# Optimization experiments

Measured on AMD Instinct MI355X. Metric: run time of the kernel, lower is better.

Reference implementation:

```python
import jax, jax.numpy as jnp
import numpy as np
from jax import lax

BN_EPS = 1e-5

def _maxpool3(x):
    # F.max_pool2d(x, 3, stride=1, padding=1): pads with -inf, window 3x3
    return lax.reduce_window(x, -jnp.inf, lax.max, (1, 1, 3, 3), (1, 1, 1, 1), 'SAME')

def _conv(x, w):
    return lax.conv_general_dilated(x, w, (1, 1), 'SAME',
                                    dimension_numbers=('NCHW', 'OIHW', 'NCHW'))

def _bn(x, g, b, m, v):
    inv = lax.rsqrt(v + BN_EPS)
    return (x - m[None, :, None, None]) * (g * inv)[None, :, None, None] + b[None, :, None, None]


def setup_inputs() -> dict:
    key = jax.random.key(0)
    ks = jax.random.split(key, 12)
    B, C, H, W = 8, 128, 160, 160
    c_ = 64  # int(c2 * 0.5)
    x = jax.random.normal(ks[0], (B, C, H, W), jnp.float32)
    fill_strength_raw = jnp.full((1, C, 1, 1), 0.5, jnp.float32)
    w1 = jax.random.normal(ks[1], (c_, C, 1, 1), jnp.float32) * 0.05
    w2 = jax.random.normal(ks[2], (c_, c_, 3, 3), jnp.float32) * 0.05
    w3 = jax.random.normal(ks[3], (C, c_, 1, 1), jnp.float32) * 0.05
    def bn_params(k, ch):
        k1, k2, k3 = jax.random.split(k, 3)
        return (jnp.ones((ch,), jnp.float32),
                jnp.zeros((ch,), jnp.float32),
                jax.random.normal(k1, (ch,), jnp.float32) * 0.1,
                jax.random.uniform(k2, (ch,), jnp.float32, 0.5, 1.5))
    g1, b1, m1, v1 = bn_params(ks[4], c_)
    g2, b2, m2, v2 = bn_params(ks[5], c_)
    g3, b3, m3, v3 = bn_params(ks[6], C)
    return dict(x=x, fill_strength_raw=fill_strength_raw,
                w1=w1, g1=g1, b1=b1, m1=m1, v1=v1,
                w2=w2, g2=g2, b2=b2, m2=m2, v2=v2,
                w3=w3, g3=g3, b3=b3, m3=m3, v3=v3)


def reference(x, fill_strength_raw,
              w1, g1, b1, m1, v1,
              w2, g2, b2, m2, v2,
              w3, g3, b3, m3, v3):
    bg_thresh_ratio, ch_sharp, ch_thresh, edge_sharp, edge_thresh = 0.3, 3.0, 0.3, 5.0, 0.5
    # AdaptiveBackgroundFill
    baseline = jnp.min(x, axis=(2, 3), keepdims=True)            # [B,C,1,1]
    local_contrast = _maxpool3(x) + _maxpool3(-x)                # max_s - min_s
    mean_contrast = jnp.mean(local_contrast, axis=(2, 3), keepdims=True) + 1e-6
    bg_mask = (local_contrast < bg_thresh_ratio * mean_contrast).astype(x.dtype)
    strength = jax.nn.sigmoid(fill_strength_raw)
    filled = x * (1.0 - strength * bg_mask) + baseline * strength * bg_mask
    # ChannelAwareEdgeEnhance_Attn
    x_abs = jnp.abs(filled)
    max_ch = jnp.max(x_abs, axis=(2, 3), keepdims=True)
    avg_ch = jnp.mean(x_abs, axis=(2, 3), keepdims=True)
    ch_weight = jax.nn.sigmoid(ch_sharp * (max_ch - avg_ch - ch_thresh))
    x_spatial = jnp.mean(x_abs, axis=1, keepdims=True)           # [B,1,H,W]
    edge = _maxpool3(x_spatial) + _maxpool3(-x_spatial)
    edge_weight = jax.nn.sigmoid(edge_sharp * (edge - edge_thresh))
    enhanced = filled * ch_weight * (1.0 + edge_weight)
    # DenseBottleneck (n=1, shortcut, c1==c2) with inference-mode BatchNorm
    o = jax.nn.silu(_bn(_conv(enhanced, w1), g1, b1, m1, v1))
    o = jax.nn.silu(_bn(_conv(o, w2), g2, b2, m2, v2))
    o = _bn(_conv(o, w3), g3, b3, m3, v3)
    out = jax.nn.silu(o + enhanced)
    # proj is Identity since c1 == c2
    return out
```

## Files before the change

### kernel.cpp

```cpp
#include <hip/hip_runtime.h>
#include <math.h>

#define BB 8
#define CC 128
#define CH 64
#define HH 160
#define WW 160
#define HW (HH*WW)
#define PP 162
#define INF __builtin_inff()

typedef __bf16 bfv8 __attribute__((ext_vector_type(8)));
typedef __bf16 bfv4 __attribute__((ext_vector_type(4)));
typedef __bf16 bfv2 __attribute__((ext_vector_type(2)));
typedef float  f4   __attribute__((ext_vector_type(4)));

__device__ __forceinline__ float sgm(float z){ return 1.0f/(1.0f + __expf(-z)); }
__device__ __forceinline__ float silu_(float z){ return z/(1.0f + __expf(-z)); }
__device__ __forceinline__ f4 MFMA(bfv8 a, bfv8 b, f4 c){
  return __builtin_amdgcn_mfma_f32_16x16x32_bf16(a, b, c, 0, 0, 0);
}

__global__ __launch_bounds__(256) void kprep2(const float* __restrict__ w1,
                                              const float* __restrict__ g1, const float* __restrict__ b1,
                                              const float* __restrict__ m1, const float* __restrict__ v1,
                                              const float* __restrict__ w2,
                                              const float* __restrict__ g2, const float* __restrict__ b2,
                                              const float* __restrict__ m2, const float* __restrict__ v2,
                                              const float* __restrict__ w3,
                                              const float* __restrict__ g3, const float* __restrict__ b3,
                                              const float* __restrict__ m3, const float* __restrict__ v3,
                                              __bf16* __restrict__ w1b, __bf16* __restrict__ w2b,
                                              __bf16* __restrict__ w3b, float* __restrict__ scsh,
                                              __bf16* __restrict__ o1p){
  int bid = blockIdx.x;
  if(bid < 64){
    int t = bid*256 + threadIdx.x;
    int stride = 64*256;
    for(int i=t; i<CH*CC; i+=stride) w1b[i] = (__bf16)w1[i];
    for(int i=t; i<CC*CH; i+=stride) w3b[i] = (__bf16)w3[i];
    for(int i=t; i<9*CH*CH; i+=stride){
      int tap = i >> 12; int rem = i & 4095; int oc = rem >> 6; int ic = rem & 63;
      w2b[i] = (__bf16)w2[(oc*CH + ic)*9 + tap];
    }
    if(t < CH){
      float s = g1[t]*rsqrtf(v1[t] + 1e-5f);
      scsh[t] = s; scsh[64+t] = b1[t] - m1[t]*s;
      float s2 = g2[t]*rsqrtf(v2[t] + 1e-5f);
      scsh[128+t] = s2; scsh[192+t] = b2[t] - m2[t]*s2;
    }
    if(t >= 64 && t < 64+CC){
      int c = t - 64;
      float s3 = g3[c]*rsqrtf(v3[c] + 1e-5f);
      scsh[256+c] = s3; scsh[384+c] = b3[c] - m3[c]*s3;
    }
  } else {
    int b = bid - 64;
    __bf16* base = o1p + (size_t)b*PP*PP*CH;
    int t = threadIdx.x;
    bfv4 z = {(__bf16)0.f,(__bf16)0.f,(__bf16)0.f,(__bf16)0.f};
    for(int i=t; i<644*16; i+=256){
      int e = i >> 4; int c4 = (i & 15)*4;
      int h, w;
      if(e < 162){ h = 0; w = e; }
      else if(e < 324){ h = 161; w = e - 162; }
      else if(e < 484){ h = e - 324 + 1; w = 0; }
      else { h = e - 484 + 1; w = 161; }
      *(bfv4*)(base + ((size_t)h*PP + w)*CH + c4) = z;
    }
  }
}

__device__ __forceinline__ void load8s(const float* __restrict__ xp, int lc,
                                       int start, float (&C)[8]){
  #pragma unroll
  for(int k=0;k<8;++k){
    int hr = start + k;
    C[k] = (hr < HH) ? xp[hr*WW + lc] : 0.f;
  }
}

__device__ __forceinline__ void proc1s(int base, const float (&C)[8],
                                       float& Mp, float& mp, float& Mc, float& mc,
                                       float& mn, float& sum){
  #pragma unroll
  for(int k=0;k<8;++k){
    int hr = base + 1 + k;
    float Lv = __shfl_up(C[k],1), Rv = __shfl_down(C[k],1);
    float Mn, mr;
    if(hr < HH){
      Mn = fmaxf(fmaxf(Lv,C[k]),Rv);
      mr = fminf(fminf(Lv,C[k]),Rv);
      mn = fminf(mn, C[k]);
    } else { Mn = -INF; mr = INF; }
    sum += fmaxf(fmaxf(Mp,Mc),Mn) - fminf(fminf(mp,mc),mr);
    Mp=Mc; mp=mc; Mc=Mn; mc=mr;
  }
}

__device__ __forceinline__ void proc2s(int base, int lc, bool act, const float (&C)[8],
                                       float& Mp, float& mp, float& Mc, float& mc,
                                       float& cen, float& amax, float& asum,
                                       float th, float basev, float s,
                                       __bf16* __restrict__ fp){
  #pragma unroll
  for(int k=0;k<8;++k){
    int hr = base + 1 + k;
    int h  = base + k;
    float Lv = __shfl_up(C[k],1), Rv = __shfl_down(C[k],1);
    float Mn, mr;
    if(hr < HH){
      Mn = fmaxf(fmaxf(Lv,C[k]),Rv);
      mr = fminf(fminf(Lv,C[k]),Rv);
    } else { Mn = -INF; mr = INF; }
    float contrast = fmaxf(fmaxf(Mp,Mc),Mn) - fminf(fminf(mp,mc),mr);
    float f = (contrast < th) ? cen*(1.f-s) + basev*s : cen;
    if(act) fp[h*WW + lc] = (__bf16)f;
    float a = fabsf(f);
    amax = fmaxf(amax, a); asum += a;
    Mp=Mc; mp=mc; Mc=Mn; mc=mr; cen = C[k];
  }
}

__global__ __launch_bounds__(192) void k12(const float* __restrict__ x,
                                           const float* __restrict__ fsr,
                                           __bf16* __restrict__ fill16,
                                           float* __restrict__ chw){
  __shared__ float ra[256], rb[256];
  __shared__ float sb[2];
  int bc = blockIdx.x;
  int c  = bc & (CC-1);
  int t  = threadIdx.x;
  int w  = t >> 6, l = t & 63;
  int oc = 62*w + l - 1;
  bool act = (l >= 1) && (l <= 62) && (oc < WW);
  int lc = oc < 0 ? 0 : (oc > WW-1 ? WW-1 : oc);
  const float* xp = x + (size_t)bc*HW;

  float CA[8], CB[8];

  float mn = INF, sum = 0.f;
  float Mp=-INF, mp=INF, Mc, mc;
  {
    float C0 = xp[lc];
    float Lv = __shfl_up(C0,1), Rv = __shfl_down(C0,1);
    Mc = fmaxf(fmaxf(Lv,C0),Rv); mc = fminf(fminf(Lv,C0),Rv);
    mn = C0;
  }
  load8s(xp, lc, 1, CA);
  for(int h0=0; h0<HH; h0+=16){
    load8s(xp, lc, h0+9, CB);
    proc1s(h0,   CA, Mp, mp, Mc, mc, mn, sum);
    if(h0+16 < HH) load8s(xp, lc, h0+17, CA);
    proc1s(h0+8, CB, Mp, mp, Mc, mc, mn, sum);
  }
  ra[t] = act ? mn : INF;
  rb[t] = act ? sum : 0.f;
  if(t < 64){ ra[192+t] = INF; rb[192+t] = 0.f; }
  __syncthreads();
  for(int s=128; s>0; s>>=1){
    if(t < s){ ra[t]=fminf(ra[t],ra[t+s]); rb[t]+=rb[t+s]; }
    __syncthreads();
  }
  if(t==0){ sb[0]=ra[0]; sb[1]=0.3f*(rb[0]/(float)HW + 1e-6f); }
  __syncthreads();
  float base = sb[0], th = sb[1];
  float s = sgm(fsr[c]);

  __bf16* fp = fill16 + (size_t)bc*HW;
  float amax=0.f, asum=0.f;
  Mp=-INF; mp=INF;
  float cen;
  {
    float C0 = xp[lc];
    float Lv = __shfl_up(C0,1), Rv = __shfl_down(C0,1);
    Mc = fmaxf(fmaxf(Lv,C0),Rv); mc = fminf(fminf(Lv,C0),Rv);
    cen = C0;
  }
  load8s(xp, lc, 1, CA);
  for(int h0=0; h0<HH; h0+=16){
    load8s(xp, lc, h0+9, CB);
    proc2s(h0,   lc, act, CA, Mp, mp, Mc, mc, cen, amax, asum, th, base, s, fp);
    if(h0+16 < HH) load8s(xp, lc, h0+17, CA);
    proc2s(h0+8, lc, act, CB, Mp, mp, Mc, mc, cen, amax, asum, th, base, s, fp);
  }
  ra[t] = act ? amax : 0.f;
  rb[t] = act ? asum : 0.f;
  if(t < 64){ ra[192+t] = 0.f; rb[192+t] = 0.f; }
  __syncthreads();
  for(int st=128; st>0; st>>=1){
    if(t < st){ ra[t]=fmaxf(ra[t],ra[t+st]); rb[t]+=rb[t+st]; }
    __syncthreads();
  }
  if(t==0) chw[bc] = sgm(3.0f*(ra[0] - rb[0]/(float)HW - 0.3f));
}

__global__ __launch_bounds__(64) void k3_xs(const __bf16* __restrict__ fill16,
                                            float* __restrict__ xs){
  int i = blockIdx.x*64 + threadIdx.x;
  int b = i / (HW/8); int p8 = (i - b*(HW/8))*8;
  const __bf16* fp = fill16 + (size_t)b*CC*HW + p8;
  float s0=0,s1=0,s2=0,s3=0,s4=0,s5=0,s6=0,s7=0;
  #pragma unroll 4
  for(int c=0; c<CC; ++c){
    bfv8 v = *(const bfv8*)(fp + (size_t)c*HW);
    s0 += fabsf((float)v[0]); s1 += fabsf((float)v[1]);
    s2 += fabsf((float)v[2]); s3 += fabsf((float)v[3]);
    s4 += fabsf((float)v[4]); s5 += fabsf((float)v[5]);
    s6 += fabsf((float)v[6]); s7 += fabsf((float)v[7]);
  }
  f4 r0 = {s0*(1.f/CC), s1*(1.f/CC), s2*(1.f/CC), s3*(1.f/CC)};
  f4 r1 = {s4*(1.f/CC), s5*(1.f/CC), s6*(1.f/CC), s7*(1.f/CC)};
  *(f4*)(xs + (size_t)b*HW + p8)     = r0;
  *(f4*)(xs + (size_t)b*HW + p8 + 4) = r1;
}

__global__ __launch_bounds__(256) void k_enh(const __bf16* __restrict__ fill16,
                                             const float* __restrict__ chw,
                                             const float* __restrict__ xs,
                                             __bf16* __restrict__ enh){
  __shared__ __bf16 tile[64][132];
  __shared__ float ewl[64];
  int b  = blockIdx.x / 400;
  int p0 = (blockIdx.x % 400) * 64;
  int t  = threadIdx.x;
  if(t < 64){
    int p = p0 + t; int h = p/WW, w = p - h*WW;
    const float* xpb = xs + (size_t)b*HW;
    int h0 = h>0?h-1:0, h1 = h<HH-1?h+1:h;
    int w0 = w>0?w-1:0, w1 = w<WW-1?w+1:w;
    float M = -INF, m = INF;
    for(int hh=h0; hh<=h1; ++hh)
      for(int ww=w0; ww<=w1; ++ww){
        float v = xpb[hh*WW+ww]; M = fmaxf(M,v); m = fminf(m,v);
      }
    ewl[t] = sgm(5.0f*((M-m) - 0.5f));
  }
  __syncthreads();
  #pragma unroll
  for(int e=0; e<8; ++e){
    int idx = e*256 + t; int ic = idx >> 4; int pp = (idx & 15)*4;
    bfv4 v = *(const bfv4*)(fill16 + ((size_t)(b*CC + ic))*HW + p0 + pp);
    float g = chw[b*CC + ic];
    #pragma unroll
    for(int i2=0;i2<4;++i2)
      tile[pp+i2][ic] = (__bf16)((float)v[i2] * g * (1.f + ewl[pp+i2]));
  }
  __syncthreads();
  #pragma unroll
  for(int e=0; e<8; ++e){
    int idx = e*256 + t; int p = idx >> 5; int icg = idx & 31;
    bfv4 v = *(const bfv4*)&tile[p][icg*4];
    *(bfv4*)&enh[((size_t)(b*HW + p0 + p))*CC + icg*4] = v;
  }
}

__global__ __launch_bounds__(256) void c1_mfma(const __bf16* __restrict__ enh,
                                               const __bf16* __restrict__ w1b,
                                               const float* __restrict__ scsh,
                                               __bf16* __restrict__ o1p){
  int lane = threadIdx.x & 63, wv = threadIdx.x >> 6;
  int u = blockIdx.x*4 + wv;
  int b = u / 320; int r = u % 320; int h = r >> 1; int w0base = (r & 1)*80;
  int q = lane >> 4, j = lane & 15;
  bfv8 afr[4][4];
  #pragma unroll
  for(int mt=0; mt<4; ++mt)
    #pragma unroll
    for(int kk=0; kk<4; ++kk)
      afr[mt][kk] = *(const bfv8*)&w1b[(mt*16 + j)*CC + kk*32 + q*8];
  f4 sc4[4], sh4[4];
  #pragma unroll
  for(int mt=0; mt<4; ++mt){
    sc4[mt] = *(const f4*)&scsh[mt*16 + q*4];
    sh4[mt] = *(const f4*)&scsh[64 + mt*16 + q*4];
  }
  const __bf16* ebase = enh + (size_t)b*HW*CC;
  __bf16* obase = o1p + (size_t)b*PP*PP*CH;
  for(int s5=0; s5<5; ++s5){
    int w0 = w0base + s5*16;
    int p0 = h*WW + w0;
    const __bf16* bp = ebase + (size_t)(p0 + j)*CC + q*8;
    bfv8 bf[4];
    #pragma unroll
    for(int kk=0; kk<4; ++kk) bf[kk] = *(const bfv8*)(bp + kk*32);
    f4 acc[4] = {{0,0,0,0},{0,0,0,0},{0,0,0,0},{0,0,0,0}};
    #pragma unroll
    for(int kk=0; kk<4; ++kk)
      #pragma unroll
      for(int mt=0; mt<4; ++mt)
        acc[mt] = MFMA(afr[mt][kk], bf[kk], acc[mt]);
    int w = w0 + j;
    __bf16* op = obase + ((size_t)(h+1)*PP + (w+1))*CH + q*4;
    #pragma unroll
    for(int mt=0; mt<4; ++mt){
      bfv4 ov;
      #pragma unroll
      for(int rr=0; rr<4; ++rr){
        float z = acc[mt][rr]*sc4[mt][rr] + sh4[mt][rr];
        ov[rr] = (__bf16)silu_(z);
      }
      *(bfv4*)(op + mt*16) = ov;
    }
  }
}

__global__ __launch_bounds__(256) void c2_mfma(const __bf16* __restrict__ o1p,
                                               const __bf16* __restrict__ w2b,
                                               const float* __restrict__ scsh,
                                               __bf16* __restrict__ o2){
  __shared__ __bf16 lds[4*82*64];
  int lane = threadIdx.x & 63, mt = threadIdx.x >> 6;
  int u = blockIdx.x;
  int b = u / 160; int r_ = u % 160; int hp = r_ >> 1; int wh = r_ & 1;
  int h0 = hp*2;
  int wstart = wh*80;
  int q = lane >> 4, j = lane & 15;
  const __bf16* ibase = o1p + (size_t)b*PP*PP*CH;
  {
    int t = threadIdx.x;
    int wvbase = t & ~63;
    #pragma unroll
    for(int it=0; it<11; ++it){
      int i = it*256 + t;
      if(i < 2624){
        int r = i / 656; int rem = i - r*656;
        int w = rem >> 3; int kp = rem & 7;
        int k = kp ^ (w & 7);
        const __bf16* src = ibase + ((size_t)(h0+r)*PP + wstart + w)*CH + k*8;
        char* dst = (char*)lds + (size_t)(it*256 + wvbase)*16;
        __builtin_amdgcn_global_load_lds((const __attribute__((address_space(1))) void*)src,
                                         (__attribute__((address_space(3))) void*)dst,
                                         16, 0, 0);
      }
    }
  }
  bfv8 afr[9][2];
  #pragma unroll
  for(int t=0; t<9; ++t)
    #pragma unroll
    for(int icb=0; icb<2; ++icb)
      afr[t][icb] = *(const bfv8*)&w2b[(t*CH + mt*16 + j)*CH + icb*32 + q*8];
  f4 sc4 = *(const f4*)&scsh[128 + mt*16 + q*4];
  f4 sh4 = *(const f4*)&scsh[192 + mt*16 + q*4];
  asm volatile("s_waitcnt vmcnt(0)" ::: "memory");
  __syncthreads();

  __bf16* obase = o2 + (size_t)b*HW*CH;
  for(int s5=0; s5<5; ++s5){
    int wb = s5*16;
    f4 a00={0,0,0,0}, a01={0,0,0,0}, a10={0,0,0,0}, a11={0,0,0,0};
    #pragma unroll
    for(int r=0; r<4; ++r){
      bfv8 bv0[3], bv1[3];
      #pragma unroll
      for(int dw=0; dw<3; ++dw){
        int wl = wb + j + dw;
        int basee = r*5248 + wl*64;
        int k0 = q ^ (wl & 7);
        bv0[dw] = *(const bfv8*)&lds[basee + k0*8];
        bv1[dw] = *(const bfv8*)&lds[basee + (k0^4)*8];
      }
      #pragma unroll
      for(int dw=0; dw<3; ++dw){
        if(r < 3){
          a00 = MFMA(afr[r*3+dw][0], bv0[dw], a00);
          a01 = MFMA(afr[r*3+dw][1], bv1[dw], a01);
        }
        if(r >= 1){
          a10 = MFMA(afr[(r-1)*3+dw][0], bv0[dw], a10);
          a11 = MFMA(afr[(r-1)*3+dw][1], bv1[dw], a11);
        }
      }
    }
    f4 acc0 = a00 + a01, acc1 = a10 + a11;
    int w0 = wstart + wb;
    __bf16* op0 = obase + ((size_t)(h0*WW + w0 + j))*CH + mt*16 + q*4;
    __bf16* op1 = obase + ((size_t)((h0+1)*WW + w0 + j))*CH + mt*16 + q*4;
    bfv4 ov0, ov1;
    #pragma unroll
    for(int rr=0; rr<4; ++rr){
      ov0[rr] = (__bf16)silu_(acc0[rr]*sc4[rr] + sh4[rr]);
      ov1[rr] = (__bf16)silu_(acc1[rr]*sc4[rr] + sh4[rr]);
    }
    *(bfv4*)op0 = ov0;
    *(bfv4*)op1 = ov1;
  }
}

__global__ __launch_bounds__(256) void c3_mfma(const __bf16* __restrict__ o2,
                                               const __bf16* __restrict__ w3b,
                                               const float* __restrict__ scsh,
                                               const __bf16* __restrict__ enh,
                                               float* __restrict__ out){
  __shared__ float ot[CC][66];
  int lane = threadIdx.x & 63, wv = threadIdx.x >> 6;
  int b = blockIdx.x / 400; int p0 = (blockIdx.x % 400)*64;
  int q = lane >> 4, j = lane & 15;
  int px0 = wv*16;
  int pix = p0 + px0 + j;
  const __bf16* bp = o2 + ((size_t)b*HW + pix)*CH + q*8;
  bfv8 bf0 = *(const bfv8*)bp;
  bfv8 bf1 = *(const bfv8*)(bp + 32);
  f4 acc[8];
  #pragma unroll
  for(int mt=0; mt<8; ++mt){
    bfv8 a0 = *(const bfv8*)&w3b[(mt*16 + j)*CH + q*8];
    bfv8 a1 = *(const bfv8*)&w3b[(mt*16 + j)*CH + 32 + q*8];
    f4 z = {0.f,0.f,0.f,0.f};
    z = MFMA(a0, bf0, z);
    z = MFMA(a1, bf1, z);
    acc[mt] = z;
  }
  const __bf16* ep = enh + ((size_t)b*HW + pix)*CC;
  #pragma unroll
  for(int mt=0; mt<8; ++mt){
    f4 scg = *(const f4*)&scsh[256 + mt*16 + q*4];
    f4 shg = *(const f4*)&scsh[384 + mt*16 + q*4];
    bfv4 e4 = *(const bfv4*)(ep + mt*16 + q*4);
    #pragma unroll
    for(int rr=0; rr<4; ++rr){
      float z = acc[mt][rr]*scg[rr] + shg[rr] + (float)e4[rr];
      ot[mt*16 + q*4 + rr][px0 + j] = silu_(z);
    }
  }
  __syncthreads();
  int t = threadIdx.x;
  #pragma unroll
  for(int e=0; e<8; ++e){
    int oc = e*16 + (t >> 4);
    int c4 = (t & 15)*4;
    f4 v = *(const f4*)&ot[oc][c4];
    *(f4*)&out[((size_t)(b*CC + oc))*HW + p0 + c4] = v;
  }
}

extern "C" void kernel_launch(void* const* d_in, const int* in_sizes, int n_in,
                              void* d_out, int out_size, void* d_ws, size_t ws_size,
                              hipStream_t stream) {
  const float* x   = (const float*)d_in[0];
  const float* fsr = (const float*)d_in[1];
  const float* w1  = (const float*)d_in[2];
  const float* g1  = (const float*)d_in[3];
  const float* b1  = (const float*)d_in[4];
  const float* m1  = (const float*)d_in[5];
  const float* v1  = (const float*)d_in[6];
  const float* w2  = (const float*)d_in[7];
  const float* g2  = (const float*)d_in[8];
  const float* b2  = (const float*)d_in[9];
  const float* m2  = (const float*)d_in[10];
  const float* v2  = (const float*)d_in[11];
  const float* w3  = (const float*)d_in[12];
  const float* g3  = (const float*)d_in[13];
  const float* b3  = (const float*)d_in[14];
  const float* m3  = (const float*)d_in[15];
  const float* v3  = (const float*)d_in[16];
  float* out = (float*)d_out;

  char* wp = (char*)d_ws;
  __bf16* fill16 = (__bf16*)wp;  wp += (size_t)BB*CC*HW*2;
  __bf16* enh    = (__bf16*)wp;  wp += (size_t)BB*HW*CC*2;
  __bf16* o1p    = (__bf16*)wp;  wp += (size_t)BB*PP*PP*CH*2;
  __bf16* o2b    = (__bf16*)wp;  wp += (size_t)BB*HW*CH*2;
  float*  xs     = (float*)wp;   wp += (size_t)BB*HW*4;
  float*  chw    = (float*)wp;   wp += 1024*4;
  __bf16* w1b    = (__bf16*)wp;  wp += (size_t)CH*CC*2;
  __bf16* w3b    = (__bf16*)wp;  wp += (size_t)CC*CH*2;
  __bf16* w2b    = (__bf16*)wp;  wp += (size_t)9*CH*CH*2;
  float*  scsh   = (float*)wp;   wp += 512*4;

  kprep2  <<<dim3(72), dim3(256), 0, stream>>>(w1,g1,b1,m1,v1, w2,g2,b2,m2,v2,
                                               w3,g3,b3,m3,v3, w1b,w2b,w3b,scsh, o1p);
  k12     <<<dim3(BB*CC), dim3(192), 0, stream>>>(x, fsr, fill16, chw);
  k3_xs   <<<dim3(400), dim3(64), 0, stream>>>(fill16, xs);
  k_enh   <<<dim3(BB*400), dim3(256), 0, stream>>>(fill16, chw, xs, enh);
  c1_mfma <<<dim3(640), dim3(256), 0, stream>>>(enh, w1b, scsh, o1p);
  c2_mfma <<<dim3(1280), dim3(256), 0, stream>>>(o1p, w2b, scsh, o2b);
  c3_mfma <<<dim3(3200), dim3(256), 0, stream>>>(o2b, w3b, scsh, enh, out);
}
```

Baseline: 193.5 us.

## Fuse enhance into conv1, recompute residual in conv3, precompute edge weights

```diff
diff --git a/kernel.cpp b/kernel.cpp
--- a/kernel.cpp
+++ b/kernel.cpp
@@ -12,13 +12,21 @@
 
 typedef __bf16 bfv8 __attribute__((ext_vector_type(8)));
 typedef __bf16 bfv4 __attribute__((ext_vector_type(4)));
-typedef __bf16 bfv2 __attribute__((ext_vector_type(2)));
 typedef float  f4   __attribute__((ext_vector_type(4)));
 
 __device__ __forceinline__ float sgm(float z){ return 1.0f/(1.0f + __expf(-z)); }
 __device__ __forceinline__ float silu_(float z){ return z/(1.0f + __expf(-z)); }
 __device__ __forceinline__ f4 MFMA(bfv8 a, bfv8 b, f4 c){
   return __builtin_amdgcn_mfma_f32_16x16x32_bf16(a, b, c, 0, 0, 0);
+}
+
+__device__ __forceinline__ float hrow3L(const float* __restrict__ r, int w,
+                                        float& hM, float& hm){
+  float cv = r[w];
+  float M = cv, m = cv;
+  if(w > 0){ float l = r[w-1]; M = fmaxf(M,l); m = fminf(m,l); }
+  if(w < WW-1){ float rr = r[w+1]; M = fmaxf(M,rr); m = fminf(m,rr); }
+  hM = M; hm = m; return cv;
 }
 
 __global__ __launch_bounds__(256) void kprep2(const float* __restrict__ w1,
@@ -215,27 +223,38 @@
   *(f4*)(xs + (size_t)b*HW + p8 + 4) = r1;
 }
 
-__global__ __launch_bounds__(256) void k_enh(const __bf16* __restrict__ fill16,
-                                             const float* __restrict__ chw,
-                                             const float* __restrict__ xs,
-                                             __bf16* __restrict__ enh){
+__global__ __launch_bounds__(256) void k4_ew(const float* __restrict__ xs,
+                                             float* __restrict__ ew){
+  int b  = blockIdx.x / 5;
+  int r0 = (blockIdx.x % 5) * 32;
+  int w  = threadIdx.x;
+  if(w >= WW) return;
+  const float* xp = xs + (size_t)b*HW;
+  float* ep = ew + (size_t)b*HW;
+  float hMp, hmp, hMc, hmc, hMn, hmn;
+  if(r0 > 0) hrow3L(xp + (r0-1)*WW, w, hMp, hmp); else { hMp=-INF; hmp=INF; }
+  hrow3L(xp + r0*WW, w, hMc, hmc);
+  #pragma unroll 4
+  for(int h=r0; h<r0+32; ++h){
+    if(h < HH-1) hrow3L(xp + (h+1)*WW, w, hMn, hmn); else { hMn=-INF; hmn=INF; }
+    float contrast = fmaxf(fmaxf(hMp,hMc),hMn) - fminf(fminf(hmp,hmc),hmn);
+    ep[h*WW + w] = sgm(5.0f*(contrast - 0.5f));
+    hMp=hMc; hmp=hmc; hMc=hMn; hmc=hmn;
+  }
+}
+
+__global__ __launch_bounds__(256) void c1f(const __bf16* __restrict__ fill16,
+                                           const float* __restrict__ chw,
+                                           const float* __restrict__ ew,
+                                           const __bf16* __restrict__ w1b,
+                                           const float* __restrict__ scsh,
+                                           __bf16* __restrict__ o1p){
   __shared__ __bf16 tile[64][132];
   __shared__ float ewl[64];
   int b  = blockIdx.x / 400;
   int p0 = (blockIdx.x % 400) * 64;
   int t  = threadIdx.x;
-  if(t < 64){
-    int p = p0 + t; int h = p/WW, w = p - h*WW;
-    const float* xpb = xs + (size_t)b*HW;
-    int h0 = h>0?h-1:0, h1 = h<HH-1?h+1:h;
-    int w0 = w>0?w-1:0, w1 = w<WW-1?w+1:w;
-    float M = -INF, m = INF;
-    for(int hh=h0; hh<=h1; ++hh)
-      for(int ww=w0; ww<=w1; ++ww){
-        float v = xpb[hh*WW+ww]; M = fmaxf(M,v); m = fminf(m,v);
-      }
-    ewl[t] = sgm(5.0f*((M-m) - 0.5f));
-  }
+  if(t < 64) ewl[t] = ew[(size_t)b*HW + p0 + t];
   __syncthreads();
   #pragma unroll
   for(int e=0; e<8; ++e){
@@ -246,22 +265,7 @@
     for(int i2=0;i2<4;++i2)
       tile[pp+i2][ic] = (__bf16)((float)v[i2] * g * (1.f + ewl[pp+i2]));
   }
-  __syncthreads();
-  #pragma unroll
-  for(int e=0; e<8; ++e){
-    int idx = e*256 + t; int p = idx >> 5; int icg = idx & 31;
-    bfv4 v = *(const bfv4*)&tile[p][icg*4];
-    *(bfv4*)&enh[((size_t)(b*HW + p0 + p))*CC + icg*4] = v;
-  }
-}
-
-__global__ __launch_bounds__(256) void c1_mfma(const __bf16* __restrict__ enh,
-                                               const __bf16* __restrict__ w1b,
-                                               const float* __restrict__ scsh,
-                                               __bf16* __restrict__ o1p){
-  int lane = threadIdx.x & 63, wv = threadIdx.x >> 6;
-  int u = blockIdx.x*4 + wv;
-  int b = u / 320; int r = u % 320; int h = r >> 1; int w0base = (r & 1)*80;
+  int lane = t & 63, wv = t >> 6;
   int q = lane >> 4, j = lane & 15;
   bfv8 afr[4][4];
   #pragma unroll
@@ -275,33 +279,28 @@
     sc4[mt] = *(const f4*)&scsh[mt*16 + q*4];
     sh4[mt] = *(const f4*)&scsh[64 + mt*16 + q*4];
   }
-  const __bf16* ebase = enh + (size_t)b*HW*CC;
-  __bf16* obase = o1p + (size_t)b*PP*PP*CH;
-  for(int s5=0; s5<5; ++s5){
-    int w0 = w0base + s5*16;
-    int p0 = h*WW + w0;
-    const __bf16* bp = ebase + (size_t)(p0 + j)*CC + q*8;
-    bfv8 bf[4];
-    #pragma unroll
-    for(int kk=0; kk<4; ++kk) bf[kk] = *(const bfv8*)(bp + kk*32);
-    f4 acc[4] = {{0,0,0,0},{0,0,0,0},{0,0,0,0},{0,0,0,0}};
-    #pragma unroll
-    for(int kk=0; kk<4; ++kk)
-      #pragma unroll
-      for(int mt=0; mt<4; ++mt)
-        acc[mt] = MFMA(afr[mt][kk], bf[kk], acc[mt]);
-    int w = w0 + j;
-    __bf16* op = obase + ((size_t)(h+1)*PP + (w+1))*CH + q*4;
-    #pragma unroll
-    for(int mt=0; mt<4; ++mt){
-      bfv4 ov;
-      #pragma unroll
-      for(int rr=0; rr<4; ++rr){
-        float z = acc[mt][rr]*sc4[mt][rr] + sh4[mt][rr];
-        ov[rr] = (__bf16)silu_(z);
-      }
-      *(bfv4*)(op + mt*16) = ov;
-    }
+  __syncthreads();
+  bfv8 bf[4];
+  #pragma unroll
+  for(int kk=0; kk<4; ++kk) bf[kk] = *(const bfv8*)&tile[wv*16 + j][kk*32 + q*8];
+  f4 acc[4] = {{0,0,0,0},{0,0,0,0},{0,0,0,0},{0,0,0,0}};
+  #pragma unroll
+  for(int kk=0; kk<4; ++kk)
+    #pragma unroll
+    for(int mt=0; mt<4; ++mt)
+      acc[mt] = MFMA(afr[mt][kk], bf[kk], acc[mt]);
+  int px = p0 + wv*16 + j;
+  int h = px / WW; int w = px - h*WW;
+  __bf16* op = o1p + (size_t)b*PP*PP*CH + ((size_t)(h+1)*PP + (w+1))*CH + q*4;
+  #pragma unroll
+  for(int mt=0; mt<4; ++mt){
+    bfv4 ov;
+    #pragma unroll
+    for(int rr=0; rr<4; ++rr){
+      float z = acc[mt][rr]*sc4[mt][rr] + sh4[mt][rr];
+      ov[rr] = (__bf16)silu_(z);
+    }
+    *(bfv4*)(op + mt*16) = ov;
   }
 }
 
@@ -391,12 +390,17 @@
 __global__ __launch_bounds__(256) void c3_mfma(const __bf16* __restrict__ o2,
                                                const __bf16* __restrict__ w3b,
                                                const float* __restrict__ scsh,
-                                               const __bf16* __restrict__ enh,
+                                               const __bf16* __restrict__ fill16,
+                                               const float* __restrict__ chw,
+                                               const float* __restrict__ ew,
                                                float* __restrict__ out){
   __shared__ float ot[CC][66];
+  __shared__ float ewl[64];
   int lane = threadIdx.x & 63, wv = threadIdx.x >> 6;
   int b = blockIdx.x / 400; int p0 = (blockIdx.x % 400)*64;
   int q = lane >> 4, j = lane & 15;
+  int t = threadIdx.x;
+  if(t < 64) ewl[t] = ew[(size_t)b*HW + p0 + t];
   int px0 = wv*16;
   int pix = p0 + px0 + j;
   const __bf16* bp = o2 + ((size_t)b*HW + pix)*CH + q*8;
@@ -412,26 +416,29 @@
     z = MFMA(a1, bf1, z);
     acc[mt] = z;
   }
-  const __bf16* ep = enh + ((size_t)b*HW + pix)*CC;
   #pragma unroll
   for(int mt=0; mt<8; ++mt){
     f4 scg = *(const f4*)&scsh[256 + mt*16 + q*4];
     f4 shg = *(const f4*)&scsh[384 + mt*16 + q*4];
-    bfv4 e4 = *(const bfv4*)(ep + mt*16 + q*4);
-    #pragma unroll
-    for(int rr=0; rr<4; ++rr){
-      float z = acc[mt][rr]*scg[rr] + shg[rr] + (float)e4[rr];
-      ot[mt*16 + q*4 + rr][px0 + j] = silu_(z);
-    }
-  }
-  __syncthreads();
-  int t = threadIdx.x;
+    #pragma unroll
+    for(int rr=0; rr<4; ++rr)
+      ot[mt*16 + q*4 + rr][px0 + j] = acc[mt][rr]*scg[rr] + shg[rr];
+  }
+  __syncthreads();
   #pragma unroll
   for(int e=0; e<8; ++e){
     int oc = e*16 + (t >> 4);
     int c4 = (t & 15)*4;
+    float cw = chw[b*CC + oc];
+    bfv4 fb = *(const bfv4*)(fill16 + ((size_t)(b*CC + oc))*HW + p0 + c4);
     f4 v = *(const f4*)&ot[oc][c4];
-    *(f4*)&out[((size_t)(b*CC + oc))*HW + p0 + c4] = v;
+    f4 r;
+    #pragma unroll
+    for(int i2=0;i2<4;++i2){
+      float res = (float)fb[i2] * cw * (1.f + ewl[c4+i2]);
+      r[i2] = silu_(v[i2] + res);
+    }
+    *(f4*)&out[((size_t)(b*CC + oc))*HW + p0 + c4] = r;
   }
 }
 
@@ -459,10 +466,10 @@
 
   char* wp = (char*)d_ws;
   __bf16* fill16 = (__bf16*)wp;  wp += (size_t)BB*CC*HW*2;
-  __bf16* enh    = (__bf16*)wp;  wp += (size_t)BB*HW*CC*2;
   __bf16* o1p    = (__bf16*)wp;  wp += (size_t)BB*PP*PP*CH*2;
   __bf16* o2b    = (__bf16*)wp;  wp += (size_t)BB*HW*CH*2;
   float*  xs     = (float*)wp;   wp += (size_t)BB*HW*4;
+  float*  ewb    = (float*)wp;   wp += (size_t)BB*HW*4;
   float*  chw    = (float*)wp;   wp += 1024*4;
   __bf16* w1b    = (__bf16*)wp;  wp += (size_t)CH*CC*2;
   __bf16* w3b    = (__bf16*)wp;  wp += (size_t)CC*CH*2;
@@ -473,8 +480,8 @@
                                                w3,g3,b3,m3,v3, w1b,w2b,w3b,scsh, o1p);
   k12     <<<dim3(BB*CC), dim3(192), 0, stream>>>(x, fsr, fill16, chw);
   k3_xs   <<<dim3(400), dim3(64), 0, stream>>>(fill16, xs);
-  k_enh   <<<dim3(BB*400), dim3(256), 0, stream>>>(fill16, chw, xs, enh);
-  c1_mfma <<<dim3(640), dim3(256), 0, stream>>>(enh, w1b, scsh, o1p);
+  k4_ew   <<<dim3(BB*5), dim3(256), 0, stream>>>(xs, ewb);
+  c1f     <<<dim3(BB*400), dim3(256), 0, stream>>>(fill16, chw, ewb, w1b, scsh, o1p);
   c2_mfma <<<dim3(1280), dim3(256), 0, stream>>>(o1p, w2b, scsh, o2b);
-  c3_mfma <<<dim3(3200), dim3(256), 0, stream>>>(o2b, w3b, scsh, enh, out);
-}
+  c3_mfma <<<dim3(3200), dim3(256), 0, stream>>>(o2b, w3b, scsh, fill16, chw, ewb, out);
+}
```

Result: slower. 207.8 us (+7.4%).
